# Performance work log

Measured on AMD Instinct MI355X. Metric: run time of the kernel, lower is better.

Reference implementation:

```python
import jax, jax.numpy as jnp
import numpy as np
from jax import lax

B, N, T, D, H, O = 64, 16, 64, 128, 256, 1  # batch, max_neighbors, time_steps, input_dim, hidden_dim, output_dim
NEG = -1e30


def gru(x, h0, Wih, Whh, bih, bhh):
    """Single-layer PyTorch-convention GRU. x:(B,T,D) h0:(B,H) -> (ys:(B,T,H), hT:(B,H))."""
    def step(h, xt):
        gi = xt @ Wih.T + bih          # (B,3H)
        gh = h @ Whh.T + bhh           # (B,3H)
        i_r, i_z, i_n = jnp.split(gi, 3, axis=-1)
        h_r, h_z, h_n = jnp.split(gh, 3, axis=-1)
        r = jax.nn.sigmoid(i_r + h_r)
        z = jax.nn.sigmoid(i_z + h_z)
        n = jnp.tanh(i_n + r * h_n)
        h_new = (1.0 - z) * n + z * h
        return h_new, h_new
    hT, ys = lax.scan(step, h0, jnp.swapaxes(x, 0, 1))
    return jnp.swapaxes(ys, 0, 1), hT


def setup_inputs() -> dict:
    key = jax.random.key(0)
    ks = jax.random.split(key, 16)
    def xavier(k, shape):
        fan_out, fan_in = shape[0], shape[1]
        std = np.sqrt(2.0 / (fan_in + fan_out))
        return jax.random.normal(k, shape, dtype=jnp.float32) * std
    inp = {
        "node_input": jax.random.normal(ks[0], (B, T, D), dtype=jnp.float32),
        "node_hidden": jnp.zeros((1, B, H), dtype=jnp.float32),
        "neighbors_input": jax.random.normal(ks[1], (B, N, T, D), dtype=jnp.float32),
        "neighbors_hidden": jnp.zeros((1, B * N, H), dtype=jnp.float32),
        "s_len": jax.random.randint(ks[2], (B,), 1, T + 1),
        # Node GRU params
        "Wih_node": xavier(ks[3], (3 * H, D)),
        "Whh_node": xavier(ks[4], (3 * H, H)),
        "bih_node": jnp.zeros((3 * H,), dtype=jnp.float32),
        "bhh_node": jnp.zeros((3 * H,), dtype=jnp.float32),
        # Neighbor GRU params
        "Wih_ngh": xavier(ks[5], (3 * H, D)),
        "Whh_ngh": xavier(ks[6], (3 * H, H)),
        "bih_ngh": jnp.zeros((3 * H,), dtype=jnp.float32),
        "bhh_ngh": jnp.zeros((3 * H,), dtype=jnp.float32),
        # Attention projections (torch Linear convention: y = x @ W.T)
        "Wq": xavier(ks[7], (H, H)),
        "Wk": xavier(ks[8], (H, H)),
        "Wv": xavier(ks[9], (H, H)),
        "Wbil": xavier(ks[10], (H, H)),
        "bbil": jnp.zeros((T,), dtype=jnp.float32),
        "Wprj": xavier(ks[11], (O, H)),
        "bprj": jnp.zeros((O,), dtype=jnp.float32),
    }
    return inp


def reference(node_input, node_hidden, neighbors_input, neighbors_hidden, s_len,
              Wih_node, Whh_node, bih_node, bhh_node,
              Wih_ngh, Whh_ngh, bih_ngh, bhh_ngh,
              Wq, Wk, Wv, Wbil, bbil, Wprj, bprj):
    # --- GRU encodes (nlayers=1) ---
    node_out, node_hT = gru(node_input, node_hidden[0], Wih_node, Whh_node, bih_node, bhh_node)  # (B,T,H)
    ngh_in = neighbors_input.reshape(B * N, T, D)
    ngh_out, ngh_hT = gru(ngh_in, neighbors_hidden[0], Wih_ngh, Whh_ngh, bih_ngh, bhh_ngh)
    ngh_out = ngh_out.reshape(B, N, T, H)

    # --- Time attention, batched over all N+1 slots (instead of python loop) ---
    kv = jnp.concatenate([node_out[:, None], ngh_out], axis=1)  # (B,M,T,H), M=N+1
    Q = node_out @ Wq.T                                          # (B,T,H) shared query for all slots
    K = kv @ Wk.T                                                # (B,M,T,H)
    V = kv @ Wv.T                                                # (B,M,T,H)
    # Bilinear score: (Q @ Wbil) @ K^T + b  -> (B,M,T,T); bbil:(T,) broadcasts on last axis
    S = jnp.einsum('bth,bmsh->bmts', Q @ Wbil, K) + bbil
    causal = jnp.triu(jnp.ones((T, T), dtype=bool), k=1)         # mask future positions
    S = jnp.where(causal, NEG, S)
    A = jax.nn.softmax(S, axis=-1)                               # (B,M,T,T); dropout=0 (eval)
    ctx = jnp.einsum('bmts,bmsh->bmth', A, V)                    # (B,M,T,H)

    # --- Output projection and sum over slots ---
    proj = ctx @ Wprj.T + bprj                                   # (B,M,T,O)
    out = jnp.sum(proj.reshape(B, N + 1, T * O), axis=1)         # (B,T*O)
    out = jnp.squeeze(out)
    return out, node_hT[None], ngh_hT[None], A
```

## Files before the change

kernel.cpp:

```cpp
#include <hip/hip_runtime.h>
#include <hip/hip_bf16.h>

#define NEGV -1e30f
typedef __attribute__((ext_vector_type(8))) short bf16x8;
typedef __attribute__((ext_vector_type(4))) float f32x4;

__device__ __forceinline__ float rcpf_(float x) { return __builtin_amdgcn_rcpf(x); }
__device__ __forceinline__ float sigmoidf_(float x) { return rcpf_(1.0f + __expf(-x)); }
__device__ __forceinline__ float tanhf_(float x) {
    float ax = fabsf(x);
    float e = __expf(-2.0f * ax);
    float t = (1.0f - e) * rcpf_(1.0f + e);
    return copysignf(t, x);
}
__device__ __forceinline__ float bf2f(unsigned short u) {
    union { float f; unsigned int i; } x; x.i = ((unsigned int)u) << 16; return x.f;
}
__device__ __forceinline__ float bfsel(uint2 v, int rg) {
    unsigned int w = (rg < 2) ? v.x : v.y;
    return bf2f((unsigned short)((rg & 1) ? (w >> 16) : (w & 0xffffu)));
}

__device__ __forceinline__ void swz_store(const float* __restrict__ src,
    __hip_bfloat16* __restrict__ dst, int idx, int kshift)
{
    int n = idx >> kshift, k = idx & ((1 << kshift) - 1);
    int nt = n >> 4, kt = k >> 5, quad = (k & 31) >> 3, pos = k & 7;
    dst[((size_t)((nt << (kshift - 5)) + kt) * 64 + quad * 16 + (n & 15)) * 8 + pos] =
        (__hip_bfloat16)src[idx];
}

__device__ __forceinline__ void swz_store_g(const float* __restrict__ src,
    __hip_bfloat16* __restrict__ dst, int idx, int kshift)
{
    int n = idx >> kshift, k = idx & ((1 << kshift) - 1);
    int gate = n >> 8, c = n & 255, w = c >> 5, half = (c >> 4) & 1;
    int tileG = w * 6 + gate * 2 + half;
    int kt = k >> 5, quad = (k & 31) >> 3, pos = k & 7;
    dst[((size_t)((tileG << (kshift - 5)) + kt) * 64 + quad * 16 + (n & 15)) * 8 + pos] =
        (__hip_bfloat16)src[idx];
}

__global__ __launch_bounds__(256) void convert_all(
    const float* __restrict__ Wih_n, const float* __restrict__ Wih_g,
    const float* __restrict__ Whh_n, const float* __restrict__ Whh_g,
    const float* __restrict__ Wk_,   const float* __restrict__ Wv_,
    const float* __restrict__ Wbil_, const float* __restrict__ Wq_,
    __hip_bfloat16* Wih_n_sw, __hip_bfloat16* Wih_g_sw,
    __hip_bfloat16* Whh_n_sw, __hip_bfloat16* Whh_g_sw,
    __hip_bfloat16* Wk_sw, __hip_bfloat16* Wv_sw, __hip_bfloat16* wqb_sw)
{
    __shared__ __align__(16) float As[32 * 68];
    __shared__ __align__(16) float Bs[32 * 68];
    if (blockIdx.x < 2816) {
        int g = blockIdx.x * 256 + threadIdx.x;
        if (g < 98304)        swz_store_g(Wih_n, Wih_n_sw, g, 7);
        else if (g < 196608)  swz_store_g(Wih_g, Wih_g_sw, g - 98304, 7);
        else if (g < 393216)  swz_store_g(Whh_n, Whh_n_sw, g - 196608, 8);
        else if (g < 589824)  swz_store_g(Whh_g, Whh_g_sw, g - 393216, 8);
        else if (g < 655360)  swz_store(Wk_,   Wk_sw,   g - 589824, 8);
        else                  swz_store(Wv_,   Wv_sw,   g - 655360, 8);
        return;
    }
    const int bx = blockIdx.x - 2816;
    const int tid = threadIdx.x, tx = tid & 15, ty = tid >> 4;
    const int rb = (bx >> 2) * 64, cb = (bx & 3) * 64;
    float acc[4][4] = {};
    for (int k0 = 0; k0 < 256; k0 += 32) {
        __syncthreads();
        for (int f = tid; f < 2048; f += 256) {
            int kk = f >> 6, r = f & 63;
            As[kk * 68 + r] = Wbil_[(size_t)(k0 + kk) * 256 + rb + r];
        }
        for (int f = tid; f < 2048; f += 256) {
            int kk = f >> 6, c = f & 63;
            Bs[kk * 68 + c] = Wq_[(size_t)(k0 + kk) * 256 + cb + c];
        }
        __syncthreads();
#pragma unroll
        for (int kk = 0; kk < 32; ++kk) {
            float4 a4 = *(const float4*)(As + kk * 68 + ty * 4);
            float4 b4 = *(const float4*)(Bs + kk * 68 + tx * 4);
            float av[4] = {a4.x, a4.y, a4.z, a4.w};
            float bv[4] = {b4.x, b4.y, b4.z, b4.w};
#pragma unroll
            for (int i = 0; i < 4; ++i)
#pragma unroll
                for (int j = 0; j < 4; ++j) acc[i][j] += av[i] * bv[j];
        }
    }
#pragma unroll
    for (int i = 0; i < 4; ++i)
#pragma unroll
        for (int j = 0; j < 4; ++j) {
            int n = rb + ty * 4 + i, k = cb + tx * 4 + j;
            int nt = n >> 4, kt = k >> 5, quad = (k & 31) >> 3, pos = k & 7;
            wqb_sw[((size_t)(nt * 8 + kt) * 64 + quad * 16 + (n & 15)) * 8 + pos] =
                (__hip_bfloat16)acc[i][j];
        }
}

__global__ __launch_bounds__(512) void gi_gemm(
    const float* __restrict__ node_input, const float* __restrict__ neighbors_input,
    const __hip_bfloat16* __restrict__ Wih_n_sw, const __hip_bfloat16* __restrict__ Wih_g_sw,
    const float* __restrict__ bih_node, const float* __restrict__ bhh_node,
    const float* __restrict__ bih_ngh,  const float* __restrict__ bhh_ngh,
    __hip_bfloat16* __restrict__ gi)
{
    __shared__ __align__(16) __hip_bfloat16 xs[16 * 136];
    const int tid = threadIdx.x, wave = tid >> 6, lane = tid & 63;
    const int quad = lane >> 4, lr = lane & 15;
    const int sblk = blockIdx.x >> 4, tc = blockIdx.x & 15;
    const bool isnode = (sblk < 4);
    const float* __restrict__ xb = isnode
        ? (node_input + (size_t)sblk * 16 * 64 * 128)
        : (neighbors_input + ((size_t)sblk * 16 - 64) * 64 * 128);
    const __hip_bfloat16* __restrict__ Wsw = isnode ? Wih_n_sw : Wih_g_sw;
    const float* __restrict__ bi = isnode ? bih_node : bih_ngh;
    const float* __restrict__ bh = isnode ? bhh_node : bhh_ngh;

    bf16x8 wfr[24];
#pragma unroll
    for (int nt = 0; nt < 6; ++nt)
#pragma unroll
        for (int kt = 0; kt < 4; ++kt)
            wfr[nt * 4 + kt] = *(const bf16x8*)(const void*)(
                Wsw + ((size_t)((wave * 6 + nt) * 4 + kt) * 64 + lane) * 8);

    float bias6[6];
#pragma unroll
    for (int tl = 0; tl < 6; ++tl) {
        int gate = tl >> 1;
        int col = gate * 256 + wave * 32 + (tl & 1) * 16 + lr;
        bias6[tl] = bi[col] + (gate < 2 ? bh[col] : 0.0f);
    }

    const int sr = tid >> 5, sc = (tid & 31) * 4;
    __hip_bfloat16* __restrict__ gout =
        gi + (size_t)((sblk * 8 + wave) * 6) * 16384 + (size_t)lane * 4;

    for (int tt = 0; tt < 4; ++tt) {
        int t = tc * 4 + tt;
        if (tt) __syncthreads();
        float4 v = *(const float4*)(xb + ((size_t)sr * 64 + t) * 128 + sc);
        __hip_bfloat16* d = xs + sr * 136 + sc;
        d[0] = (__hip_bfloat16)v.x; d[1] = (__hip_bfloat16)v.y;
        d[2] = (__hip_bfloat16)v.z; d[3] = (__hip_bfloat16)v.w;
        __syncthreads();

        bf16x8 afr[4];
#pragma unroll
        for (int kt = 0; kt < 4; ++kt)
            afr[kt] = *(const bf16x8*)(const void*)(xs + lr * 136 + kt * 32 + quad * 8);

#pragma unroll
        for (int tl = 0; tl < 6; ++tl) {
            f32x4 acc = {0.f, 0.f, 0.f, 0.f};
#pragma unroll
            for (int kt = 0; kt < 4; ++kt)
                acc = __builtin_amdgcn_mfma_f32_16x16x32_bf16(afr[kt], wfr[tl * 4 + kt], acc, 0, 0, 0);
            union { __hip_bfloat16 p[4]; uint2 u; } pu;
#pragma unroll
            for (int rg = 0; rg < 4; ++rg) pu.p[rg] = (__hip_bfloat16)(acc[rg] + bias6[tl]);
            *(uint2*)(void*)(gout + (size_t)tl * 16384 + (size_t)t * 256) = pu.u;
        }
    }
}

__global__ __launch_bounds__(512, 2) void scan_kernel(
    const __hip_bfloat16* __restrict__ gi,
    const __hip_bfloat16* __restrict__ Whh_n_sw,
    const __hip_bfloat16* __restrict__ Whh_g_sw,
    const float* __restrict__ bhh_node, const float* __restrict__ bhh_ngh,
    const float* __restrict__ node_hidden, const float* __restrict__ neighbors_hidden,
    __hip_bfloat16* __restrict__ node_out, __hip_bfloat16* __restrict__ ngh_out,
    float* __restrict__ out_node_hT, float* __restrict__ out_ngh_hT)
{
    __shared__ __align__(16) __hip_bfloat16 wlds[96 * 64 * 8];
    __shared__ __align__(16) __hip_bfloat16 hfr[2 * 4096];
    const int tid = threadIdx.x;
    const int wave = tid >> 6, lane = tid & 63;
    const int quad = lane >> 4, lr = lane & 15;
    const int row0 = blockIdx.x * 16;
    const bool isnode = (row0 < 64);
    const __hip_bfloat16* __restrict__ Wsw = isnode ? Whh_n_sw : Whh_g_sw;
    const float* __restrict__ bhh = isnode ? bhh_node : bhh_ngh;

    bf16x8 wreg[36];
#pragma unroll
    for (int nt = 0; nt < 6; ++nt)
#pragma unroll
        for (int kt = 0; kt < 6; ++kt)
            wreg[nt * 6 + kt] = *(const bf16x8*)(const void*)(
                Wsw + ((size_t)((wave * 6 + nt) * 8 + kt) * 64 + lane) * 8);

    for (int f = tid; f < 6144; f += 512) {
        int chunk = f >> 6, l = f & 63;
        int tileG = chunk >> 1, s = chunk & 1;
        *(uint4*)(void*)(wlds + ((size_t)chunk * 64 + l) * 8) =
            *(const uint4*)(const void*)(Wsw + ((size_t)(tileG * 8 + 6 + s) * 64 + l) * 8);
    }

    const __hip_bfloat16* __restrict__ gbase =
        gi + (size_t)((blockIdx.x * 8 + wave) * 6) * 16384 + (size_t)lane * 4;

    const float bhn0 = bhh[512 + wave * 32 + lr];
    const float bhn1 = bhh[512 + wave * 32 + 16 + lr];

    const int hwoff = (wave * 64 + (lr >> 3) * 16 + quad * 4) * 8 + (lr & 7);
    float hreg[8];
    {
        const float* hsrc = isnode ? (node_hidden + (size_t)row0 * 256)
                                   : (neighbors_hidden + (size_t)(row0 - 64) * 256);
#pragma unroll
        for (int half = 0; half < 2; ++half)
#pragma unroll
            for (int rg = 0; rg < 4; ++rg) {
                float v = hsrc[(size_t)(quad * 4 + rg) * 256 + wave * 32 + half * 16 + lr];
                hreg[half * 4 + rg] = v;
                hfr[hwoff + half * 256 + rg * 8] = (__hip_bfloat16)v;
            }
    }

    __hip_bfloat16* optr;
    {
        int orow = tid & 15;
        int ocol = (tid >> 6) * 32 + ((tid >> 4) & 3) * 8;
        optr = isnode ? (node_out + ((size_t)(row0 + orow) * 64) * 256 + ocol)
                      : (ngh_out + ((size_t)(row0 - 64 + orow) * 64) * 256 + ocol);
    }

    uint2 gv[6];
#pragma unroll
    for (int tl = 0; tl < 6; ++tl)
        gv[tl] = *(const uint2*)(const void*)(gbase + (size_t)tl * 16384);

    __syncthreads();

#pragma unroll 1
    for (int t = 0; t < 64; ++t) {
        const __hip_bfloat16* hr = hfr + (t & 1) * 4096;

        const int tp = (t < 63) ? (t + 1) : 63;
        uint2 gvn[6];
#pragma unroll
        for (int tl = 0; tl < 6; ++tl)
            gvn[tl] = *(const uint2*)(const void*)(gbase + (size_t)tl * 16384 + tp * 256);

        if (t) {
            uint4 ov = *(const uint4*)(const void*)(hr + tid * 8);
            *(uint4*)(void*)optr = ov;
            optr += 256;
        }

        f32x4 acc[6] = {{0.f,0.f,0.f,0.f},{0.f,0.f,0.f,0.f},{0.f,0.f,0.f,0.f},
                        {0.f,0.f,0.f,0.f},{0.f,0.f,0.f,0.f},{0.f,0.f,0.f,0.f}};
        {
#pragma unroll
            for (int kt = 0; kt < 3; ++kt) {
                bf16x8 av = *(const bf16x8*)(const void*)(hr + (kt * 64 + lane) * 8);
#pragma unroll
                for (int tl = 0; tl < 6; ++tl)
                    acc[tl] = __builtin_amdgcn_mfma_f32_16x16x32_bf16(av, wreg[tl * 6 + kt], acc[tl], 0, 0, 0);
            }
        }
        {
#pragma unroll
            for (int kt = 3; kt < 6; ++kt) {
                bf16x8 av = *(const bf16x8*)(const void*)(hr + (kt * 64 + lane) * 8);
#pragma unroll
                for (int tl = 0; tl < 6; ++tl)
                    acc[tl] = __builtin_amdgcn_mfma_f32_16x16x32_bf16(av, wreg[tl * 6 + kt], acc[tl], 0, 0, 0);
            }
        }
        {
#pragma unroll
            for (int s = 0; s < 2; ++s) {
                bf16x8 av = *(const bf16x8*)(const void*)(hr + ((6 + s) * 64 + lane) * 8);
#pragma unroll
                for (int tl = 0; tl < 6; ++tl) {
                    bf16x8 bfr = *(const bf16x8*)(const void*)(
                        wlds + ((size_t)((wave * 6 + tl) * 2 + s) * 64 + lane) * 8);
                    acc[tl] = __builtin_amdgcn_mfma_f32_16x16x32_bf16(av, bfr, acc[tl], 0, 0, 0);
                }
            }
        }

        __hip_bfloat16* hw = hfr + ((t + 1) & 1) * 4096 + hwoff;
#pragma unroll
        for (int half = 0; half < 2; ++half) {
            const float bhn = half ? bhn1 : bhn0;
#pragma unroll
            for (int rg = 0; rg < 4; ++rg) {
                float ghr = acc[half][rg];
                float ghz = acc[2 + half][rg];
                float ghn = acc[4 + half][rg] + bhn;
                float gir = bfsel(gv[half], rg);
                float giz = bfsel(gv[2 + half], rg);
                float gin = bfsel(gv[4 + half], rg);
                float r = sigmoidf_(gir + ghr);
                float z = sigmoidf_(giz + ghz);
                float n = tanhf_(gin + r * ghn);
                float hn = (1.0f - z) * n + z * hreg[half * 4 + rg];
                hreg[half * 4 + rg] = hn;
                hw[half * 256 + rg * 8] = (__hip_bfloat16)hn;
            }
        }
#pragma unroll
        for (int tl = 0; tl < 6; ++tl) gv[tl] = gvn[tl];

        asm volatile("s_waitcnt lgkmcnt(0)" ::: "memory");
        __builtin_amdgcn_s_barrier();
        __builtin_amdgcn_sched_barrier(0);
    }

    {
        uint4 ov = *(const uint4*)(const void*)(hfr + tid * 8);
        *(uint4*)(void*)optr = ov;
    }
    {
        float* hdst = isnode ? (out_node_hT + (size_t)row0 * 256)
                             : (out_ngh_hT + (size_t)(row0 - 64) * 256);
#pragma unroll
        for (int half = 0; half < 2; ++half)
#pragma unroll
            for (int rg = 0; rg < 4; ++rg)
                hdst[(size_t)(quad * 4 + rg) * 256 + wave * 32 + half * 16 + lr] = hreg[half * 4 + rg];
    }
}

__global__ __launch_bounds__(256) void kv_gemm(
    const __hip_bfloat16* __restrict__ A0, const __hip_bfloat16* __restrict__ A1,
    const __hip_bfloat16* __restrict__ Wk_sw, const __hip_bfloat16* __restrict__ Wv_sw,
    const __hip_bfloat16* __restrict__ wqb_sw,
    __hip_bfloat16* __restrict__ Kb, __hip_bfloat16* __restrict__ Vt,
    __hip_bfloat16* __restrict__ Qb)
{
    __shared__ __align__(16) __hip_bfloat16 As[64 * 264];
    const int tid = threadIdx.x, wave = tid >> 6, lane = tid & 63;
    const int quad = lane >> 4, lr = lane & 15;
    const int rb = blockIdx.x * 64;
    const bool node = rb < 4096;
    const __hip_bfloat16* A = node ? (A0 + (size_t)rb * 256) : (A1 + (size_t)(rb - 4096) * 256);

    for (int f = tid; f < 2048; f += 256) {
        int row = f >> 5, cc = (f & 31) * 8;
        *(uint4*)(void*)(As + row * 264 + cc) =
            *(const uint4*)(const void*)(A + (size_t)row * 256 + cc);
    }
    __syncthreads();

    bf16x8 afr[8];
#pragma unroll
    for (int kt = 0; kt < 8; ++kt)
        afr[kt] = *(const bf16x8*)(const void*)(As + (wave * 16 + lr) * 264 + kt * 32 + quad * 8);

    int b_, slot;
    if (node) { b_ = rb >> 6; slot = 0; }
    else { int rr = (rb - 4096) >> 6; b_ = rr >> 4; slot = (rr & 15) + 1; }
    const size_t kbase = ((size_t)b_ * 1088 + slot * 64) * 256;
    const size_t vtbase = (size_t)(b_ * 17 + slot) * 256 * 64;
    const int s0 = wave * 16 + quad * 4;

    for (int ntg = 0; ntg < 16; ++ntg) {
        f32x4 acc = {0.f, 0.f, 0.f, 0.f};
#pragma unroll
        for (int kt = 0; kt < 8; ++kt) {
            bf16x8 bfr = *(const bf16x8*)(const void*)(Wk_sw + ((size_t)(ntg * 8 + kt) * 64 + lane) * 8);
            acc = __builtin_amdgcn_mfma_f32_16x16x32_bf16(afr[kt], bfr, acc, 0, 0, 0);
        }
        int col = ntg * 16 + lr;
#pragma unroll
        for (int rg = 0; rg < 4; ++rg)
            Kb[kbase + (size_t)(s0 + rg) * 256 + col] = (__hip_bfloat16)acc[rg];
    }
    {
        const int kt2 = wave >> 1;
        const int lp = ((wave & 1) * 2 + (quad >> 1)) * 16 + lr;
        const int j0 = (quad & 1) * 4;
        for (int ntg = 0; ntg < 16; ++ntg) {
            f32x4 acc = {0.f, 0.f, 0.f, 0.f};
#pragma unroll
            for (int kt = 0; kt < 8; ++kt) {
                bf16x8 bfr = *(const bf16x8*)(const void*)(Wv_sw + ((size_t)(ntg * 8 + kt) * 64 + lane) * 8);
                acc = __builtin_amdgcn_mfma_f32_16x16x32_bf16(afr[kt], bfr, acc, 0, 0, 0);
            }
            __hip_bfloat16 t4[4];
#pragma unroll
            for (int rg = 0; rg < 4; ++rg) t4[rg] = (__hip_bfloat16)acc[rg];
            *(uint2*)(void*)(Vt + vtbase + (size_t)(((ntg * 2 + kt2) * 64 + lp) * 8 + j0)) =
                *(const uint2*)(const void*)t4;
        }
    }
    if (node) {
        for (int ntg = 0; ntg < 16; ++ntg) {
            f32x4 acc = {0.f, 0.f, 0.f, 0.f};
#pragma unroll
            for (int kt = 0; kt < 8; ++kt) {
                bf16x8 bfr = *(const bf16x8*)(const void*)(wqb_sw + ((size_t)(ntg * 8 + kt) * 64 + lane) * 8);
                acc = __builtin_amdgcn_mfma_f32_16x16x32_bf16(afr[kt], bfr, acc, 0, 0, 0);
            }
            int col = ntg * 16 + lr;
#pragma unroll
            for (int rg = 0; rg < 4; ++rg)
                Qb[(size_t)(rb + s0 + rg) * 256 + col] = (__hip_bfloat16)acc[rg];
        }
    }
}

__global__ __launch_bounds__(256) void attn_kernel(
    const __hip_bfloat16* __restrict__ Qb, const __hip_bfloat16* __restrict__ Kb,
    const __hip_bfloat16* __restrict__ Vt, const float* __restrict__ bbil,
    const float* __restrict__ Wprj, const float* __restrict__ bprj,
    float* __restrict__ A_out, float* __restrict__ out)
{
    __shared__ __align__(16) float Sbuf[64 * 68];
    __shared__ __align__(16) __hip_bfloat16 Pb[64 * 72];
    __shared__ float rowmax[64], rowrcp[64];
    __shared__ float red[64 * 16];
    const int tid = threadIdx.x;
    const int wave = tid >> 6, lane = tid & 63;
    const int quad = lane >> 4, lr = lane & 15;
    const int bm = blockIdx.x, b = bm / 17, m = bm % 17;
    const __hip_bfloat16* Qrow = Qb + (size_t)b * 64 * 256;
    const __hip_bfloat16* Krow = Kb + ((size_t)b * 1088 + m * 64) * 256;
    const __hip_bfloat16* Vtrow = Vt + (size_t)(b * 17 + m) * 256 * 64;

    f32x4 sacc[4] = {{0.f,0.f,0.f,0.f},{0.f,0.f,0.f,0.f},{0.f,0.f,0.f,0.f},{0.f,0.f,0.f,0.f}};
#pragma unroll
    for (int kt = 0; kt < 8; ++kt) {
        bf16x8 afr = *(const bf16x8*)(const void*)(Qrow + (size_t)(wave * 16 + lr) * 256 + kt * 32 + quad * 8);
#pragma unroll
        for (int c = 0; c < 4; ++c) {
            bf16x8 bfr = *(const bf16x8*)(const void*)(Krow + (size_t)(c * 16 + lr) * 256 + kt * 32 + quad * 8);
            sacc[c] = __builtin_amdgcn_mfma_f32_16x16x32_bf16(afr, bfr, sacc[c], 0, 0, 0);
        }
    }
#pragma unroll
    for (int c = 0; c < 4; ++c)
#pragma unroll
        for (int rg = 0; rg < 4; ++rg) {
            int t_ = wave * 16 + quad * 4 + rg, s_ = c * 16 + lr;
            Sbuf[t_ * 68 + s_] = (s_ <= t_) ? (sacc[c][rg] + bbil[s_]) : NEGV;
        }
    __syncthreads();
    if (tid < 64) {
        float mx = -3.0e38f;
        for (int s = 0; s < 64; ++s) mx = fmaxf(mx, Sbuf[tid * 68 + s]);
        float sum = 0.0f;
        for (int s = 0; s < 64; ++s) sum += __expf(Sbuf[tid * 68 + s] - mx);
        rowmax[tid] = mx;
        rowrcp[tid] = 1.0f / sum;
    }
    __syncthreads();
    for (int idx = tid; idx < 4096; idx += 256) {
        int t_ = idx >> 6, s_ = idx & 63;
        float e = __expf(Sbuf[t_ * 68 + s_] - rowmax[t_]) * rowrcp[t_];
        A_out[(size_t)bm * 4096 + idx] = e;
        Pb[t_ * 72 + s_] = (__hip_bfloat16)e;
    }
    __syncthreads();

    bf16x8 pfr[2];
#pragma unroll
    for (int k2 = 0; k2 < 2; ++k2)
        pfr[k2] = *(const bf16x8*)(const void*)(Pb + (wave * 16 + lr) * 72 + k2 * 32 + quad * 8);
    float part[4] = {0.f, 0.f, 0.f, 0.f};
#pragma unroll
    for (int nt = 0; nt < 16; ++nt) {
        f32x4 cacc = {0.f, 0.f, 0.f, 0.f};
#pragma unroll
        for (int k2 = 0; k2 < 2; ++k2) {
            bf16x8 bfr = *(const bf16x8*)(const void*)(Vtrow + (size_t)((nt * 2 + k2) * 64 + lane) * 8);
            cacc = __builtin_amdgcn_mfma_f32_16x16x32_bf16(pfr[k2], bfr, cacc, 0, 0, 0);
        }
        float wp = Wprj[nt * 16 + lr];
#pragma unroll
        for (int rg = 0; rg < 4; ++rg) part[rg] += cacc[rg] * wp;
    }
#pragma unroll
    for (int rg = 0; rg < 4; ++rg) red[(wave * 16 + quad * 4 + rg) * 16 + lr] = part[rg];
    __syncthreads();
    if (tid < 64) {
        float s = 0.0f;
#pragma unroll
        for (int q = 0; q < 16; ++q) s += red[tid * 16 + q];
        if (m == 0) s += 17.0f * bprj[0];
        atomicAdd(out + b * 64 + tid, s);
    }
}

extern "C" void kernel_launch(void* const* d_in, const int* in_sizes, int n_in,
                              void* d_out, int out_size, void* d_ws, size_t ws_size,
                              hipStream_t stream)
{
    const float* node_input       = (const float*)d_in[0];
    const float* node_hidden      = (const float*)d_in[1];
    const float* neighbors_input  = (const float*)d_in[2];
    const float* neighbors_hidden = (const float*)d_in[3];
    const float* Wih_node = (const float*)d_in[5];
    const float* Whh_node = (const float*)d_in[6];
    const float* bih_node = (const float*)d_in[7];
    const float* bhh_node = (const float*)d_in[8];
    const float* Wih_ngh  = (const float*)d_in[9];
    const float* Whh_ngh  = (const float*)d_in[10];
    const float* bih_ngh  = (const float*)d_in[11];
    const float* bhh_ngh  = (const float*)d_in[12];
    const float* Wq   = (const float*)d_in[13];
    const float* Wk   = (const float*)d_in[14];
    const float* Wv   = (const float*)d_in[15];
    const float* Wbil = (const float*)d_in[16];
    const float* bbil = (const float*)d_in[17];
    const float* Wprj = (const float*)d_in[18];
    const float* bprj = (const float*)d_in[19];

    float* out         = (float*)d_out;
    float* out_node_hT = out + 4096;
    float* out_ngh_hT  = out + 20480;
    float* out_A       = out + 282624;

    char* w = (char*)d_ws;
    __hip_bfloat16* Wih_n_sw = (__hip_bfloat16*)(w + 262144);
    __hip_bfloat16* Wih_g_sw = (__hip_bfloat16*)(w + 458752);
    __hip_bfloat16* Whh_n_sw = (__hip_bfloat16*)(w + 655360);
    __hip_bfloat16* Whh_g_sw = (__hip_bfloat16*)(w + 1048576);
    __hip_bfloat16* Wk_sw    = (__hip_bfloat16*)(w + 1441792);
    __hip_bfloat16* Wv_sw    = (__hip_bfloat16*)(w + 1572864);
    __hip_bfloat16* wqb_sw   = (__hip_bfloat16*)(w + 1703936);
    __hip_bfloat16* node_out_b = (__hip_bfloat16*)(w + 1835008);
    __hip_bfloat16* ngh_out_b  = (__hip_bfloat16*)(w + 3932160);
    __hip_bfloat16* qb_b       = (__hip_bfloat16*)(w + 37486592);
    __hip_bfloat16* gi         = (__hip_bfloat16*)(w + 39583744);
    __hip_bfloat16* kbuf = gi;
    __hip_bfloat16* vtbuf = kbuf + 17825792;

    hipMemsetAsync(d_out, 0, 4096 * sizeof(float), stream);

    convert_all<<<2832, 256, 0, stream>>>(
        Wih_node, Wih_ngh, Whh_node, Whh_ngh, Wk, Wv, Wbil, Wq,
        Wih_n_sw, Wih_g_sw, Whh_n_sw, Whh_g_sw, Wk_sw, Wv_sw, wqb_sw);

    gi_gemm<<<1088, 512, 0, stream>>>(
        node_input, neighbors_input, Wih_n_sw, Wih_g_sw,
        bih_node, bhh_node, bih_ngh, bhh_ngh, gi);

    scan_kernel<<<68, 512, 0, stream>>>(gi, Whh_n_sw, Whh_g_sw,
        bhh_node, bhh_ngh, node_hidden, neighbors_hidden,
        node_out_b, ngh_out_b, out_node_hT, out_ngh_hT);

    kv_gemm<<<1088, 256, 0, stream>>>(
        node_out_b, ngh_out_b, Wk_sw, Wv_sw, wqb_sw, kbuf, vtbuf, qb_b);

    attn_kernel<<<1088, 256, 0, stream>>>(qb_b, kbuf, vtbuf, bbil, Wprj, bprj,
                                          out_A, out);
}
```

Before: 423.3 us.

## Fuse K/V projection into attention kernel, keep K and V in shared memory

The K and V projections move from the separate kv_gemm kernel into the attention kernel. K and V are computed per (batch, slot) block and stored in a shared-memory buffer, which is reused first for K and then for transposed V, so the large global K/V intermediates are never written and read back. Q is now produced by its own small 64-block kernel. Each attention block now does more MFMA work and holds more LDS, which may reduce occupancy.

```diff
diff --git a/kernel.cpp b/kernel.cpp
--- a/kernel.cpp
+++ b/kernel.cpp
@@ -329,19 +329,16 @@
     }
 }
 
-__global__ __launch_bounds__(256) void kv_gemm(
-    const __hip_bfloat16* __restrict__ A0, const __hip_bfloat16* __restrict__ A1,
-    const __hip_bfloat16* __restrict__ Wk_sw, const __hip_bfloat16* __restrict__ Wv_sw,
+__global__ __launch_bounds__(256) void q_gemm(
+    const __hip_bfloat16* __restrict__ A0,
     const __hip_bfloat16* __restrict__ wqb_sw,
-    __hip_bfloat16* __restrict__ Kb, __hip_bfloat16* __restrict__ Vt,
     __hip_bfloat16* __restrict__ Qb)
 {
     __shared__ __align__(16) __hip_bfloat16 As[64 * 264];
     const int tid = threadIdx.x, wave = tid >> 6, lane = tid & 63;
     const int quad = lane >> 4, lr = lane & 15;
     const int rb = blockIdx.x * 64;
-    const bool node = rb < 4096;
-    const __hip_bfloat16* A = node ? (A0 + (size_t)rb * 256) : (A1 + (size_t)(rb - 4096) * 256);
+    const __hip_bfloat16* A = A0 + (size_t)rb * 256;
 
     for (int f = tid; f < 2048; f += 256) {
         int row = f >> 5, cc = (f & 31) * 8;
@@ -355,65 +352,30 @@
     for (int kt = 0; kt < 8; ++kt)
         afr[kt] = *(const bf16x8*)(const void*)(As + (wave * 16 + lr) * 264 + kt * 32 + quad * 8);
 
-    int b_, slot;
-    if (node) { b_ = rb >> 6; slot = 0; }
-    else { int rr = (rb - 4096) >> 6; b_ = rr >> 4; slot = (rr & 15) + 1; }
-    const size_t kbase = ((size_t)b_ * 1088 + slot * 64) * 256;
-    const size_t vtbase = (size_t)(b_ * 17 + slot) * 256 * 64;
     const int s0 = wave * 16 + quad * 4;
-
     for (int ntg = 0; ntg < 16; ++ntg) {
         f32x4 acc = {0.f, 0.f, 0.f, 0.f};
 #pragma unroll
         for (int kt = 0; kt < 8; ++kt) {
-            bf16x8 bfr = *(const bf16x8*)(const void*)(Wk_sw + ((size_t)(ntg * 8 + kt) * 64 + lane) * 8);
+            bf16x8 bfr = *(const bf16x8*)(const void*)(wqb_sw + ((size_t)(ntg * 8 + kt) * 64 + lane) * 8);
             acc = __builtin_amdgcn_mfma_f32_16x16x32_bf16(afr[kt], bfr, acc, 0, 0, 0);
         }
         int col = ntg * 16 + lr;
 #pragma unroll
         for (int rg = 0; rg < 4; ++rg)
-            Kb[kbase + (size_t)(s0 + rg) * 256 + col] = (__hip_bfloat16)acc[rg];
-    }
-    {
-        const int kt2 = wave >> 1;
-        const int lp = ((wave & 1) * 2 + (quad >> 1)) * 16 + lr;
-        const int j0 = (quad & 1) * 4;
-        for (int ntg = 0; ntg < 16; ++ntg) {
-            f32x4 acc = {0.f, 0.f, 0.f, 0.f};
-#pragma unroll
-            for (int kt = 0; kt < 8; ++kt) {
-                bf16x8 bfr = *(const bf16x8*)(const void*)(Wv_sw + ((size_t)(ntg * 8 + kt) * 64 + lane) * 8);
-                acc = __builtin_amdgcn_mfma_f32_16x16x32_bf16(afr[kt], bfr, acc, 0, 0, 0);
-            }
-            __hip_bfloat16 t4[4];
-#pragma unroll
-            for (int rg = 0; rg < 4; ++rg) t4[rg] = (__hip_bfloat16)acc[rg];
-            *(uint2*)(void*)(Vt + vtbase + (size_t)(((ntg * 2 + kt2) * 64 + lp) * 8 + j0)) =
-                *(const uint2*)(const void*)t4;
-        }
-    }
-    if (node) {
-        for (int ntg = 0; ntg < 16; ++ntg) {
-            f32x4 acc = {0.f, 0.f, 0.f, 0.f};
-#pragma unroll
-            for (int kt = 0; kt < 8; ++kt) {
-                bf16x8 bfr = *(const bf16x8*)(const void*)(wqb_sw + ((size_t)(ntg * 8 + kt) * 64 + lane) * 8);
-                acc = __builtin_amdgcn_mfma_f32_16x16x32_bf16(afr[kt], bfr, acc, 0, 0, 0);
-            }
-            int col = ntg * 16 + lr;
-#pragma unroll
-            for (int rg = 0; rg < 4; ++rg)
-                Qb[(size_t)(rb + s0 + rg) * 256 + col] = (__hip_bfloat16)acc[rg];
-        }
-    }
-}
-
-__global__ __launch_bounds__(256) void attn_kernel(
-    const __hip_bfloat16* __restrict__ Qb, const __hip_bfloat16* __restrict__ Kb,
-    const __hip_bfloat16* __restrict__ Vt, const float* __restrict__ bbil,
+            Qb[(size_t)(rb + s0 + rg) * 256 + col] = (__hip_bfloat16)acc[rg];
+    }
+}
+
+__global__ __launch_bounds__(256) void attn_fused(
+    const __hip_bfloat16* __restrict__ node_out_b,
+    const __hip_bfloat16* __restrict__ ngh_out_b,
+    const __hip_bfloat16* __restrict__ Wk_sw, const __hip_bfloat16* __restrict__ Wv_sw,
+    const __hip_bfloat16* __restrict__ Qb, const float* __restrict__ bbil,
     const float* __restrict__ Wprj, const float* __restrict__ bprj,
     float* __restrict__ A_out, float* __restrict__ out)
 {
+    __shared__ __align__(16) __hip_bfloat16 KA[64 * 264];
     __shared__ __align__(16) float Sbuf[64 * 68];
     __shared__ __align__(16) __hip_bfloat16 Pb[64 * 72];
     __shared__ float rowmax[64], rowrcp[64];
@@ -422,18 +384,52 @@
     const int wave = tid >> 6, lane = tid & 63;
     const int quad = lane >> 4, lr = lane & 15;
     const int bm = blockIdx.x, b = bm / 17, m = bm % 17;
+    const __hip_bfloat16* __restrict__ A = (m == 0)
+        ? (node_out_b + (size_t)b * 64 * 256)
+        : (ngh_out_b + ((size_t)(b * 16 + m - 1) * 64) * 256);
+
+    for (int f = tid; f < 2048; f += 256) {
+        int row = f >> 5, cc = (f & 31) * 8;
+        *(uint4*)(void*)(KA + row * 264 + cc) =
+            *(const uint4*)(const void*)(A + (size_t)row * 256 + cc);
+    }
+    __syncthreads();
+
+    bf16x8 afr[8];
+#pragma unroll
+    for (int kt = 0; kt < 8; ++kt)
+        afr[kt] = *(const bf16x8*)(const void*)(KA + (wave * 16 + lr) * 264 + kt * 32 + quad * 8);
     const __hip_bfloat16* Qrow = Qb + (size_t)b * 64 * 256;
-    const __hip_bfloat16* Krow = Kb + ((size_t)b * 1088 + m * 64) * 256;
-    const __hip_bfloat16* Vtrow = Vt + (size_t)(b * 17 + m) * 256 * 64;
+    bf16x8 qfr[8];
+#pragma unroll
+    for (int kt = 0; kt < 8; ++kt)
+        qfr[kt] = *(const bf16x8*)(const void*)(Qrow + (size_t)(wave * 16 + lr) * 256 + kt * 32 + quad * 8);
+    __syncthreads();
+
+    {
+        const int s0 = wave * 16 + quad * 4;
+        for (int ntg = 0; ntg < 16; ++ntg) {
+            f32x4 acc = {0.f, 0.f, 0.f, 0.f};
+#pragma unroll
+            for (int kt = 0; kt < 8; ++kt) {
+                bf16x8 bfr = *(const bf16x8*)(const void*)(Wk_sw + ((size_t)(ntg * 8 + kt) * 64 + lane) * 8);
+                acc = __builtin_amdgcn_mfma_f32_16x16x32_bf16(afr[kt], bfr, acc, 0, 0, 0);
+            }
+            int col = ntg * 16 + lr;
+#pragma unroll
+            for (int rg = 0; rg < 4; ++rg)
+                KA[(s0 + rg) * 264 + col] = (__hip_bfloat16)acc[rg];
+        }
+    }
+    __syncthreads();
 
     f32x4 sacc[4] = {{0.f,0.f,0.f,0.f},{0.f,0.f,0.f,0.f},{0.f,0.f,0.f,0.f},{0.f,0.f,0.f,0.f}};
 #pragma unroll
     for (int kt = 0; kt < 8; ++kt) {
-        bf16x8 afr = *(const bf16x8*)(const void*)(Qrow + (size_t)(wave * 16 + lr) * 256 + kt * 32 + quad * 8);
 #pragma unroll
         for (int c = 0; c < 4; ++c) {
-            bf16x8 bfr = *(const bf16x8*)(const void*)(Krow + (size_t)(c * 16 + lr) * 256 + kt * 32 + quad * 8);
-            sacc[c] = __builtin_amdgcn_mfma_f32_16x16x32_bf16(afr, bfr, sacc[c], 0, 0, 0);
+            bf16x8 bfr = *(const bf16x8*)(const void*)(KA + (c * 16 + lr) * 264 + kt * 32 + quad * 8);
+            sacc[c] = __builtin_amdgcn_mfma_f32_16x16x32_bf16(qfr[kt], bfr, sacc[c], 0, 0, 0);
         }
     }
 #pragma unroll
@@ -444,6 +440,25 @@
             Sbuf[t_ * 68 + s_] = (s_ <= t_) ? (sacc[c][rg] + bbil[s_]) : NEGV;
         }
     __syncthreads();
+
+    {
+        const int kt2 = wave >> 1;
+        const int lp = ((wave & 1) * 2 + (quad >> 1)) * 16 + lr;
+        const int j0 = (quad & 1) * 4;
+        for (int ntg = 0; ntg < 16; ++ntg) {
+            f32x4 acc = {0.f, 0.f, 0.f, 0.f};
+#pragma unroll
+            for (int kt = 0; kt < 8; ++kt) {
+                bf16x8 bfr = *(const bf16x8*)(const void*)(Wv_sw + ((size_t)(ntg * 8 + kt) * 64 + lane) * 8);
+                acc = __builtin_amdgcn_mfma_f32_16x16x32_bf16(afr[kt], bfr, acc, 0, 0, 0);
+            }
+            __hip_bfloat16 t4[4];
+#pragma unroll
+            for (int rg = 0; rg < 4; ++rg) t4[rg] = (__hip_bfloat16)acc[rg];
+            *(uint2*)(void*)(KA + (size_t)(((ntg * 2 + kt2) * 64 + lp) * 8 + j0)) =
+                *(const uint2*)(const void*)t4;
+        }
+    }
     if (tid < 64) {
         float mx = -3.0e38f;
         for (int s = 0; s < 64; ++s) mx = fmaxf(mx, Sbuf[tid * 68 + s]);
@@ -453,6 +468,7 @@
         rowrcp[tid] = 1.0f / sum;
     }
     __syncthreads();
+
     for (int idx = tid; idx < 4096; idx += 256) {
         int t_ = idx >> 6, s_ = idx & 63;
         float e = __expf(Sbuf[t_ * 68 + s_] - rowmax[t_]) * rowrcp[t_];
@@ -471,7 +487,7 @@
         f32x4 cacc = {0.f, 0.f, 0.f, 0.f};
 #pragma unroll
         for (int k2 = 0; k2 < 2; ++k2) {
-            bf16x8 bfr = *(const bf16x8*)(const void*)(Vtrow + (size_t)((nt * 2 + k2) * 64 + lane) * 8);
+            bf16x8 bfr = *(const bf16x8*)(const void*)(KA + (size_t)((nt * 2 + k2) * 64 + lane) * 8);
             cacc = __builtin_amdgcn_mfma_f32_16x16x32_bf16(pfr[k2], bfr, cacc, 0, 0, 0);
         }
         float wp = Wprj[nt * 16 + lr];
@@ -531,8 +547,6 @@
     __hip_bfloat16* ngh_out_b  = (__hip_bfloat16*)(w + 3932160);
     __hip_bfloat16* qb_b       = (__hip_bfloat16*)(w + 37486592);
     __hip_bfloat16* gi         = (__hip_bfloat16*)(w + 39583744);
-    __hip_bfloat16* kbuf = gi;
-    __hip_bfloat16* vtbuf = kbuf + 17825792;
 
     hipMemsetAsync(d_out, 0, 4096 * sizeof(float), stream);
 
@@ -548,9 +562,9 @@
         bhh_node, bhh_ngh, node_hidden, neighbors_hidden,
         node_out_b, ngh_out_b, out_node_hT, out_ngh_hT);
 
-    kv_gemm<<<1088, 256, 0, stream>>>(
-        node_out_b, ngh_out_b, Wk_sw, Wv_sw, wqb_sw, kbuf, vtbuf, qb_b);
-
-    attn_kernel<<<1088, 256, 0, stream>>>(qb_b, kbuf, vtbuf, bbil, Wprj, bprj,
-                                          out_A, out);
-}
+    q_gemm<<<64, 256, 0, stream>>>(node_out_b, wqb_sw, qb_b);
+
+    attn_fused<<<1088, 256, 0, stream>>>(
+        node_out_b, ngh_out_b, Wk_sw, Wv_sw, qb_b, bbil, Wprj, bprj,
+        out_A, out);
+}
```

Measured after the change: 404.9 us. -4.3%, faster.
